# Kernel tuning notes

Measured on AMD Instinct MI355X. Metric: run time of the kernel, lower is better.

The kernel has to match this reference:

```python
import jax, jax.numpy as jnp
import numpy as np

DIM = 1024
N_HEADS = 16
HEAD_DIM = 64
SEQ = 2048
BATCH = 2


def setup_inputs() -> dict:
    key = jax.random.key(0)
    ks = jax.random.split(key, 7)
    scale = 1.0 / np.sqrt(DIM)
    return {
        "q": jax.random.normal(ks[0], (BATCH, SEQ, DIM), dtype=jnp.float32),
        "k": jax.random.normal(ks[1], (BATCH, SEQ, DIM), dtype=jnp.float32),
        "v": jax.random.normal(ks[2], (BATCH, SEQ, DIM), dtype=jnp.float32),
        "wq": jax.random.normal(ks[3], (DIM, DIM), dtype=jnp.float32) * scale,
        "wk": jax.random.normal(ks[4], (DIM, DIM), dtype=jnp.float32) * scale,
        "wv": jax.random.normal(ks[5], (DIM, DIM), dtype=jnp.float32) * scale,
        "wo": jax.random.normal(ks[6], (DIM, DIM), dtype=jnp.float32) * scale,
    }


def reference(q, k, v, wq, wk, wv, wo):
    B, S, D = q.shape
    # Linear layers: y = x @ W.T (torch nn.Linear convention)
    qh = (q @ wq.T).reshape(B, S, N_HEADS, HEAD_DIM).transpose(0, 2, 1, 3)  # [B,H,S,hd]
    kh = (k @ wk.T).reshape(B, S, N_HEADS, HEAD_DIM).transpose(0, 2, 1, 3)
    vh = (v @ wv.T).reshape(B, S, N_HEADS, HEAD_DIM).transpose(0, 2, 1, 3)
    score = jnp.einsum('bhqd,bhkd->bhqk', qh, kh) / jnp.sqrt(jnp.float32(HEAD_DIM))
    # causal mask: upper triangle (j > i) set to -inf
    causal = jnp.tril(jnp.ones((S, S), dtype=bool))
    score = jnp.where(causal[None, None], score, -jnp.inf)
    attn = jax.nn.softmax(score, axis=-1)
    out = jnp.einsum('bhqk,bhkd->bhqd', attn, vh)  # [B,H,S,hd]
    out = out.transpose(0, 2, 1, 3).reshape(B, S, D)
    return out @ wo.T
```

## Files before the change

### kernel.cpp

```cpp
#include <hip/hip_runtime.h>

typedef unsigned short u16;
typedef unsigned int   u32;
typedef __bf16 bf16x8 __attribute__((ext_vector_type(8)));
typedef float  f32x4  __attribute__((ext_vector_type(4)));
typedef unsigned short u16x4 __attribute__((ext_vector_type(4)));
typedef unsigned short u16x8 __attribute__((ext_vector_type(8)));
typedef unsigned int   u32x2 __attribute__((ext_vector_type(2)));
typedef unsigned int   u32x4 __attribute__((ext_vector_type(4)));

#define DIM   1024
#define SEQ   2048
#define NH    16
#define HD    64
#define NBATCH 2

#define NEG_INF (-__builtin_inff())
#define QSCALE 0.1803368801111204f


__device__ __forceinline__ u16 f2bf(float f) {
  unsigned u = __float_as_uint(f);
  unsigned r = (u + 0x7FFFu + ((u >> 16) & 1u)) >> 16;
  return (u16)r;
}

__device__ __forceinline__ u32 pkbf(float a, float b) {
#if __has_builtin(__builtin_amdgcn_cvt_pk_bf16_f32)
  typedef __bf16 bf16x2 __attribute__((ext_vector_type(2)));
  bf16x2 t = __builtin_amdgcn_cvt_pk_bf16_f32(a, b);
  return __builtin_bit_cast(u32, t);
#else
  return (u32)f2bf(a) | ((u32)f2bf(b) << 16);
#endif
}

__device__ __forceinline__ void gload16(const void* g, void* lds_uniform) {
  __builtin_amdgcn_global_load_lds(
      (__attribute__((address_space(1))) void*)(size_t)g,
      (__attribute__((address_space(3))) void*)lds_uniform,
      16, 0, 0);
}


__global__ __launch_bounds__(256) void cvt_all(
    const float* __restrict__ q, const float* __restrict__ k, const float* __restrict__ v,
    const float* __restrict__ wq, const float* __restrict__ wk, const float* __restrict__ wv,
    const float* __restrict__ wo, u16* __restrict__ ws) {
  const size_t M = 1u << 20;
  int b = blockIdx.x;
  const float* src;
  u16* dst;
  int idx;
  if (b < 6144) {
    int t = b >> 11; idx = b & 2047;
    src = (t == 0) ? q : (t == 1) ? k : v;
    dst = ws + (size_t)t * 4 * M;
  } else {
    int t = (b - 6144) >> 9; idx = (b - 6144) & 511;
    src = (t == 0) ? wq : (t == 1) ? wk : (t == 2) ? wv : wo;
    dst = ws + (12 + (size_t)t) * M;
  }
  size_t i = ((size_t)idx * 256 + threadIdx.x) * 8;
  float4 a = *(const float4*)(src + i);
  float4 c = *(const float4*)(src + i + 4);
  u16x8 o;
  o[0] = f2bf(a.x); o[1] = f2bf(a.y); o[2] = f2bf(a.z); o[3] = f2bf(a.w);
  o[4] = f2bf(c.x); o[5] = f2bf(c.y); o[6] = f2bf(c.z); o[7] = f2bf(c.w);
  *(u16x8*)(dst + i) = o;
}


__device__ __forceinline__ void gemm128_core(const u16* __restrict__ A,
                                             const u16* __restrict__ W,
                                             int bm, int bn,
                                             u16* lds, f32x4 (&acc)[4][4]) {
  const int K = 1024;
  const int tid = threadIdx.x;
  const int wave = tid >> 6, lane = tid & 63;
  const int quad = lane >> 4, l15 = lane & 15;
  const int warp_m = wave >> 1, warp_n = wave & 1;

  const int c0 = wave * 128 + lane, c1 = c0 + 64;
  const u16* Ag0 = A + (size_t)(bm * 128 + (c0 >> 2)) * K + (c0 & 3) * 8;
  const u16* Ag1 = A + (size_t)(bm * 128 + (c1 >> 2)) * K + (c1 & 3) * 8;
  const u16* Wg0 = W + (size_t)(bn * 128 + (c0 >> 2)) * K + (c0 & 3) * 8;
  const u16* Wg1 = W + (size_t)(bn * 128 + (c1 >> 2)) * K + (c1 & 3) * 8;
  const int lA0 = (wave * 2 + 0) * 512;
  const int lA1 = (wave * 2 + 1) * 512;
  const int lB0 = 4096 + (wave * 2 + 0) * 512;
  const int lB1 = 4096 + (wave * 2 + 1) * 512;

  gload16(Ag0, lds + lA0);
  gload16(Ag1, lds + lA1);
  gload16(Wg0, lds + lB0);
  gload16(Wg1, lds + lB1);

  for (int k0 = 0; k0 < K; k0 += 32) {
    const int buf = (k0 >> 5) & 1;
    u16* cur = lds + buf * 8192;
    __syncthreads();
    if (k0 + 32 < K) {
      u16* nxt = lds + (buf ^ 1) * 8192;
      gload16(Ag0 + k0 + 32, nxt + lA0);
      gload16(Ag1 + k0 + 32, nxt + lA1);
      gload16(Wg0 + k0 + 32, nxt + lB0);
      gload16(Wg1 + k0 + 32, nxt + lB1);
    }

    bf16x8 af[4], bfr[4];
#pragma unroll
    for (int i = 0; i < 4; ++i) {
      af[i]  = *(const bf16x8*)(cur + (warp_m * 64 + i * 16 + l15) * 32 + quad * 8);
      bfr[i] = *(const bf16x8*)(cur + 4096 + (warp_n * 64 + i * 16 + l15) * 32 + quad * 8);
    }
#pragma unroll
    for (int i = 0; i < 4; ++i)
#pragma unroll
      for (int j = 0; j < 4; ++j)
        acc[i][j] = __builtin_amdgcn_mfma_f32_16x16x32_bf16(af[i], bfr[j], acc[i][j], 0, 0, 0);
  }
}

__global__ __launch_bounds__(256) void gemm_qkv(
    const u16* __restrict__ qb, const u16* __restrict__ kb, const u16* __restrict__ vb,
    const u16* __restrict__ wq, const u16* __restrict__ wk, const u16* __restrict__ wv,
    u16* __restrict__ Qo, u16* __restrict__ Ko, u16* __restrict__ Vt) {
  __shared__ __align__(16) u16 lds[2][8192];
  const int id = blockIdx.x;
  const int c = id & 7, bn = (id >> 3) & 7, t = id >> 6;
  const int g = c + 8 * t;
  const int bm = g & 31, z = g >> 5;

  const u16* A = (z == 0) ? qb : (z == 1) ? kb : vb;
  const u16* W = (z == 0) ? wq : (z == 1) ? wk : wv;
  f32x4 acc[4][4] = {};
  gemm128_core(A, W, bm, bn, &lds[0][0], acc);

  const int tid = threadIdx.x;
  const int wave = tid >> 6, lane = tid & 63;
  const int quad = lane >> 4, l15 = lane & 15;
  const int warp_m = wave >> 1, warp_n = wave & 1;
#pragma unroll
  for (int i = 0; i < 4; ++i)
#pragma unroll
    for (int j = 0; j < 4; ++j) {
      int s0 = bm * 128 + warp_m * 64 + i * 16 + quad * 4;
      int n  = bn * 128 + warp_n * 64 + j * 16 + l15;
      int bb = s0 >> 11, sl0 = s0 & 2047, h = n >> 6, d = n & 63;
      if (z == 2) {
        int ssw = (sl0 & ~63) | ((((sl0 >> 3) & 7) ^ (d & 7)) << 3) | (sl0 & 7);
        u16x4 pv;
        pv[0] = f2bf(acc[i][j][0]); pv[1] = f2bf(acc[i][j][1]);
        pv[2] = f2bf(acc[i][j][2]); pv[3] = f2bf(acc[i][j][3]);
        *(u16x4*)(Vt + ((size_t)(bb * NH + h) * HD + d) * SEQ + ssw) = pv;
      } else if (z == 1) {
#pragma unroll
        for (int r = 0; r < 4; ++r) {
          int s = sl0 + r;
          int dsw = (((d >> 3) ^ (s & 7)) << 3) | (d & 7);
          Ko[((size_t)(bb * NH + h) * SEQ + s) * HD + dsw] = f2bf(acc[i][j][r]);
        }
      } else {
#pragma unroll
        for (int r = 0; r < 4; ++r)
          Qo[((size_t)(bb * NH + h) * SEQ + sl0 + r) * HD + d] = f2bf(acc[i][j][r] * QSCALE);
      }
    }
}

__global__ __launch_bounds__(256) void gemm_out(
    const u16* __restrict__ A, const u16* __restrict__ W, float* __restrict__ Out) {
  __shared__ __align__(16) u16 lds[2][8192];
  const int id = blockIdx.x;
  const int bn = (id >> 3) & 7;
  const int bm = (id & 7) + 8 * (id >> 6);
  f32x4 acc[4][4] = {};
  gemm128_core(A, W, bm, bn, &lds[0][0], acc);

  const int tid = threadIdx.x;
  const int wave = tid >> 6, lane = tid & 63;
  const int quad = lane >> 4, l15 = lane & 15;
  const int warp_m = wave >> 1, warp_n = wave & 1;
#pragma unroll
  for (int i = 0; i < 4; ++i)
#pragma unroll
    for (int j = 0; j < 4; ++j)
#pragma unroll
      for (int r = 0; r < 4; ++r) {
        int m = bm * 128 + warp_m * 64 + i * 16 + quad * 4 + r;
        int n = bn * 128 + warp_n * 64 + j * 16 + l15;
        Out[(size_t)m * DIM + n] = acc[i][j][r];
      }
}


__global__ __launch_bounds__(256) void attn_kernel(
    const u16* __restrict__ Q, const u16* __restrict__ K,
    const u16* __restrict__ Vt, u16* __restrict__ O) {
  __shared__ __align__(16) u16 Kl[2][4096];
  __shared__ __align__(16) u16 Vl[2][4096];
  __shared__ __align__(16) u32 Plm[4][512];
  const int tid = threadIdx.x;
  const int wave = tid >> 6, lane = tid & 63;
  const int quad = lane >> 4, l15 = lane & 15;
  const int bx = blockIdx.x;
  const int bh = bx & 31;
  const int qt = 31 - (bx >> 5);
  const int b = bh >> 4, h = bh & 15;

  const u16* qbase = Q + ((size_t)bh * SEQ + qt * 64 + wave * 16 + l15) * HD + quad * 8;
  const bf16x8 qf0 = *(const bf16x8*)(qbase);
  const bf16x8 qf1 = *(const bf16x8*)(qbase + 32);

  f32x4 o[4] = {};
  float l_sum = 0.f, m_run = NEG_INF;

  const int c0 = wave * 128 + lane, c1 = c0 + 64;
  const u16* Ksrc = K + (size_t)bh * SEQ * HD;
  const u16* Vsrc = Vt + (size_t)bh * HD * SEQ;
  const int sw0 = ((quad ^ (l15 & 7)) << 3);
  const int sw1 = (((4 + quad) ^ (l15 & 7)) << 3);

  {
    gload16(Ksrc + (size_t)c0 * 8, &Kl[0][(wave * 2 + 0) * 512]);
    gload16(Ksrc + (size_t)c1 * 8, &Kl[0][(wave * 2 + 1) * 512]);
    gload16(Vsrc + (size_t)(c0 >> 3) * SEQ + (c0 & 7) * 8, &Vl[0][(wave * 2 + 0) * 512]);
    gload16(Vsrc + (size_t)(c1 >> 3) * SEQ + (c1 & 7) * 8, &Vl[0][(wave * 2 + 1) * 512]);
  }

  u32* prow = &Plm[wave][l15 * 32];
  const int psw = l15 & 7;
  const int phalf = (quad & 1) * 2, pbhi = quad >> 1;

  for (int kt = 0; kt <= qt; ++kt) {
    const int buf = kt & 1;
    __syncthreads();
    if (kt < qt) {
      const int nb = buf ^ 1;
      const size_t kb = (size_t)(kt + 1) * 64;
      gload16(Ksrc + (kb * HD) + (size_t)c0 * 8, &Kl[nb][(wave * 2 + 0) * 512]);
      gload16(Ksrc + (kb * HD) + (size_t)c1 * 8, &Kl[nb][(wave * 2 + 1) * 512]);
      gload16(Vsrc + (size_t)(c0 >> 3) * SEQ + kb + (c0 & 7) * 8, &Vl[nb][(wave * 2 + 0) * 512]);
      gload16(Vsrc + (size_t)(c1 >> 3) * SEQ + kb + (c1 & 7) * 8, &Vl[nb][(wave * 2 + 1) * 512]);
    }

    f32x4 s[4];
#pragma unroll
    for (int kn = 0; kn < 4; ++kn) {
      const u16* arow = &Kl[buf][(kn * 16 + l15) * 64];
      bf16x8 kf0 = *(const bf16x8*)(arow + sw0);
      bf16x8 kf1 = *(const bf16x8*)(arow + sw1);
      f32x4 z = {};
      z = __builtin_amdgcn_mfma_f32_16x16x32_bf16(kf0, qf0, z, 0, 0, 0);
      z = __builtin_amdgcn_mfma_f32_16x16x32_bf16(kf1, qf1, z, 0, 0, 0);
      s[kn] = z;
    }

    if (kt == qt) {
      const int qloc = wave * 16 + l15;
#pragma unroll
      for (int kn = 0; kn < 4; ++kn)
#pragma unroll
        for (int r = 0; r < 4; ++r)
          if (kn * 16 + quad * 4 + r > qloc) s[kn][r] = NEG_INF;
    }

    float mr = NEG_INF;
#pragma unroll
    for (int kn = 0; kn < 4; ++kn)
#pragma unroll
      for (int r = 0; r < 4; ++r) mr = fmaxf(mr, s[kn][r]);
    mr = fmaxf(mr, __shfl_xor(mr, 16));
    mr = fmaxf(mr, __shfl_xor(mr, 32));
    const float mnew = fmaxf(m_run, mr);
    const float alpha = __builtin_amdgcn_exp2f(m_run - mnew);
    m_run = mnew;
    float rs = 0.f;
#pragma unroll
    for (int kn = 0; kn < 4; ++kn)
#pragma unroll
      for (int r = 0; r < 4; ++r) {
        float p = __builtin_amdgcn_exp2f(s[kn][r] - mnew);
        s[kn][r] = p;
        rs += p;
      }
    rs += __shfl_xor(rs, 16);
    rs += __shfl_xor(rs, 32);
    l_sum = l_sum * alpha + rs;

#pragma unroll
    for (int n = 0; n < 4; ++n)
#pragma unroll
      for (int r = 0; r < 4; ++r) o[n][r] *= alpha;

#pragma unroll
    for (int kn = 0; kn < 4; ++kn) {
      u32x2 w;
      w[0] = pkbf(s[kn][0], s[kn][1]);
      w[1] = pkbf(s[kn][2], s[kn][3]);
      *(u32x2*)(prow + (((2 * kn + pbhi) ^ psw) << 2) + phalf) = w;
    }
    u32x4 t0 = *(const u32x4*)(prow + ((quad ^ psw) << 2));
    u32x4 t1 = *(const u32x4*)(prow + (((4 + quad) ^ psw) << 2));
    bf16x8 pf0 = __builtin_bit_cast(bf16x8, t0);
    bf16x8 pf1 = __builtin_bit_cast(bf16x8, t1);

#pragma unroll
    for (int n = 0; n < 4; ++n) {
      const u16* vrow = &Vl[buf][(n * 16 + l15) * 64];
      bf16x8 vf0 = *(const bf16x8*)(vrow + sw0);
      bf16x8 vf1 = *(const bf16x8*)(vrow + sw1);
      o[n] = __builtin_amdgcn_mfma_f32_16x16x32_bf16(vf0, pf0, o[n], 0, 0, 0);
      o[n] = __builtin_amdgcn_mfma_f32_16x16x32_bf16(vf1, pf1, o[n], 0, 0, 0);
    }
  }

  const float inv = 1.f / l_sum;
  const int srow = qt * 64 + wave * 16 + l15;
  u16* obase = O + ((size_t)b * SEQ + srow) * DIM + h * HD + quad * 4;
#pragma unroll
  for (int n = 0; n < 4; ++n) {
    u32x2 st;
    st[0] = pkbf(o[n][0] * inv, o[n][1] * inv);
    st[1] = pkbf(o[n][2] * inv, o[n][3] * inv);
    *(u32x2*)(obase + n * 16) = st;
  }
}


extern "C" void kernel_launch(void* const* d_in, const int* in_sizes, int n_in,
                              void* d_out, int out_size, void* d_ws, size_t ws_size,
                              hipStream_t stream) {
  (void)in_sizes; (void)n_in; (void)out_size; (void)ws_size;
  const float* q  = (const float*)d_in[0];
  const float* k  = (const float*)d_in[1];
  const float* v  = (const float*)d_in[2];
  const float* wq = (const float*)d_in[3];
  const float* wk = (const float*)d_in[4];
  const float* wv = (const float*)d_in[5];
  const float* wo = (const float*)d_in[6];

  u16* ws = (u16*)d_ws;
  const size_t EL = 1u << 20;
  u16* QB = ws + 0 * EL;
  u16* KB = ws + 4 * EL;
  u16* VB = ws + 8 * EL;
  u16* WQ = ws + 12 * EL;
  u16* WK = ws + 13 * EL;
  u16* WV = ws + 14 * EL;
  u16* WO = ws + 15 * EL;
  u16* Qw = ws + 16 * EL;
  u16* Kw = ws + 20 * EL;
  u16* Vtw = ws + 24 * EL;
  u16* AO = ws + 28 * EL;

  cvt_all<<<8192, 256, 0, stream>>>(q, k, v, wq, wk, wv, wo, ws);
  gemm_qkv<<<768, 256, 0, stream>>>(QB, KB, VB, WQ, WK, WV, Qw, Kw, Vtw);
  attn_kernel<<<1024, 256, 0, stream>>>(Qw, Kw, Vtw, AO);
  gemm_out<<<256, 256, 0, stream>>>(AO, WO, (float*)d_out);
}
```

Before: 202.4 us.

## Permute V layout to feed P from registers and compute row sums via MFMA

The V projection epilogue now writes V^T with a sequence permutation that matches the register layout of the softmax probabilities. This lets the attention kernel pack P straight into MFMA operands and drop the per-iteration LDS round trip through the Plm buffer. The softmax denominator now comes from an extra MFMA against a vector of ones, which also removes the shuffle reductions. The cost is two more MFMAs per tile and a row sum taken from bf16-rounded probabilities, which changes numerics slightly.

After: 200.6 us. No clear change (-0.9%).

```diff
diff --git a/kernel.cpp b/kernel.cpp
--- a/kernel.cpp
+++ b/kernel.cpp
@@ -149,11 +149,12 @@
       int n  = bn * 128 + warp_n * 64 + j * 16 + l15;
       int bb = s0 >> 11, sl0 = s0 & 2047, h = n >> 6, d = n & 63;
       if (z == 2) {
-        int ssw = (sl0 & ~63) | ((((sl0 >> 3) & 7) ^ (d & 7)) << 3) | (sl0 & 7);
+        int pos = (sl0 & ~63) | (sl0 & 32) | ((sl0 & 12) << 1) | ((sl0 & 16) >> 2);
+        int psw = (pos & ~63) | ((((pos >> 3) & 7) ^ (d & 7)) << 3) | (pos & 7);
         u16x4 pv;
         pv[0] = f2bf(acc[i][j][0]); pv[1] = f2bf(acc[i][j][1]);
         pv[2] = f2bf(acc[i][j][2]); pv[3] = f2bf(acc[i][j][3]);
-        *(u16x4*)(Vt + ((size_t)(bb * NH + h) * HD + d) * SEQ + ssw) = pv;
+        *(u16x4*)(Vt + ((size_t)(bb * NH + h) * HD + d) * SEQ + psw) = pv;
       } else if (z == 1) {
 #pragma unroll
         for (int r = 0; r < 4; ++r) {
@@ -200,7 +201,7 @@
     const u16* __restrict__ Vt, u16* __restrict__ O) {
   __shared__ __align__(16) u16 Kl[2][4096];
   __shared__ __align__(16) u16 Vl[2][4096];
-  __shared__ __align__(16) u32 Plm[4][512];
+
   const int tid = threadIdx.x;
   const int wave = tid >> 6, lane = tid & 63;
   const int quad = lane >> 4, l15 = lane & 15;
@@ -213,8 +214,13 @@
   const bf16x8 qf0 = *(const bf16x8*)(qbase);
   const bf16x8 qf1 = *(const bf16x8*)(qbase + 32);
 
+  bf16x8 ones;
+#pragma unroll
+  for (int i = 0; i < 8; ++i) ones[i] = (__bf16)1.0f;
+
   f32x4 o[4] = {};
-  float l_sum = 0.f, m_run = NEG_INF;
+  f32x4 o4 = {};
+  float m_run = NEG_INF;
 
   const int c0 = wave * 128 + lane, c1 = c0 + 64;
   const u16* Ksrc = K + (size_t)bh * SEQ * HD;
@@ -228,10 +234,6 @@
     gload16(Vsrc + (size_t)(c0 >> 3) * SEQ + (c0 & 7) * 8, &Vl[0][(wave * 2 + 0) * 512]);
     gload16(Vsrc + (size_t)(c1 >> 3) * SEQ + (c1 & 7) * 8, &Vl[0][(wave * 2 + 1) * 512]);
   }
-
-  u32* prow = &Plm[wave][l15 * 32];
-  const int psw = l15 & 7;
-  const int phalf = (quad & 1) * 2, pbhi = quad >> 1;
 
   for (int kt = 0; kt <= qt; ++kt) {
     const int buf = kt & 1;
@@ -276,35 +278,29 @@
     const float mnew = fmaxf(m_run, mr);
     const float alpha = __builtin_amdgcn_exp2f(m_run - mnew);
     m_run = mnew;
-    float rs = 0.f;
 #pragma unroll
     for (int kn = 0; kn < 4; ++kn)
 #pragma unroll
-      for (int r = 0; r < 4; ++r) {
-        float p = __builtin_amdgcn_exp2f(s[kn][r] - mnew);
-        s[kn][r] = p;
-        rs += p;
-      }
-    rs += __shfl_xor(rs, 16);
-    rs += __shfl_xor(rs, 32);
-    l_sum = l_sum * alpha + rs;
-
-#pragma unroll
-    for (int n = 0; n < 4; ++n)
-#pragma unroll
-      for (int r = 0; r < 4; ++r) o[n][r] *= alpha;
-
-#pragma unroll
-    for (int kn = 0; kn < 4; ++kn) {
-      u32x2 w;
-      w[0] = pkbf(s[kn][0], s[kn][1]);
-      w[1] = pkbf(s[kn][2], s[kn][3]);
-      *(u32x2*)(prow + (((2 * kn + pbhi) ^ psw) << 2) + phalf) = w;
-    }
-    u32x4 t0 = *(const u32x4*)(prow + ((quad ^ psw) << 2));
-    u32x4 t1 = *(const u32x4*)(prow + (((4 + quad) ^ psw) << 2));
+      for (int r = 0; r < 4; ++r)
+        s[kn][r] = __builtin_amdgcn_exp2f(s[kn][r] - mnew);
+
+    u32x4 t0, t1;
+    t0[0] = pkbf(s[0][0], s[0][1]); t0[1] = pkbf(s[0][2], s[0][3]);
+    t0[2] = pkbf(s[1][0], s[1][1]); t0[3] = pkbf(s[1][2], s[1][3]);
+    t1[0] = pkbf(s[2][0], s[2][1]); t1[1] = pkbf(s[2][2], s[2][3]);
+    t1[2] = pkbf(s[3][0], s[3][1]); t1[3] = pkbf(s[3][2], s[3][3]);
     bf16x8 pf0 = __builtin_bit_cast(bf16x8, t0);
     bf16x8 pf1 = __builtin_bit_cast(bf16x8, t1);
+
+#pragma unroll
+    for (int n = 0; n < 4; ++n)
+#pragma unroll
+      for (int r = 0; r < 4; ++r) o[n][r] *= alpha;
+#pragma unroll
+    for (int r = 0; r < 4; ++r) o4[r] *= alpha;
+
+    o4 = __builtin_amdgcn_mfma_f32_16x16x32_bf16(ones, pf0, o4, 0, 0, 0);
+    o4 = __builtin_amdgcn_mfma_f32_16x16x32_bf16(ones, pf1, o4, 0, 0, 0);
 
 #pragma unroll
     for (int n = 0; n < 4; ++n) {
@@ -316,7 +312,7 @@
     }
   }
 
-  const float inv = 1.f / l_sum;
+  const float inv = 1.f / o4[0];
   const int srow = qt * 64 + wave * 16 + l15;
   u16* obase = O + ((size_t)b * SEQ + srow) * DIM + h * HD + quad * 4;
 #pragma unroll
```
